# Kernel tuning notes

Hardware: AMD Instinct MI355X
Metric: run time of the kernel (lower is better)

The kernel has to match this reference:

```python
import jax, jax.numpy as jnp
import numpy as np

C_IN = 256
C_INTER = 128  # in_channels // reduction
B, H, W = 8, 64, 64


def setup_inputs() -> dict:
    key = jax.random.key(0)
    ks = jax.random.split(key, 9)
    s_in = 1.0 / np.sqrt(C_IN)
    s_int = 1.0 / np.sqrt(C_INTER)
    return {
        "x": jax.random.normal(ks[0], (B, C_IN, H, W), dtype=jnp.float32),
        "Wg": jax.random.uniform(ks[1], (C_INTER, C_IN), jnp.float32, -s_in, s_in),
        "bg": jax.random.uniform(ks[2], (C_INTER,), jnp.float32, -s_in, s_in),
        "Wt": jax.random.uniform(ks[3], (C_INTER, C_IN), jnp.float32, -s_in, s_in),
        "bt": jax.random.uniform(ks[4], (C_INTER,), jnp.float32, -s_in, s_in),
        "Wp": jax.random.uniform(ks[5], (C_INTER, C_IN), jnp.float32, -s_in, s_in),
        "bp": jax.random.uniform(ks[6], (C_INTER,), jnp.float32, -s_in, s_in),
        "Wo": jax.random.uniform(ks[7], (C_IN, C_INTER), jnp.float32, -s_int, s_int),
        "bo": jax.random.uniform(ks[8], (C_IN,), jnp.float32, -s_int, s_int),
    }


def reference(x, Wg, bg, Wt, bt, Wp, bp, Wo, bo):
    n, C, h, w = x.shape
    xf = x.reshape(n, C, h * w)                      # [n, C, L]
    # 1x1 convs == per-pixel linear projections
    g = jnp.einsum('dc,ncl->nld', Wg, xf) + bg       # [n, L, ci]
    th = jnp.einsum('dc,ncl->nld', Wt, xf) + bt      # [n, L, ci]
    ph = jnp.einsum('dc,ncl->ndl', Wp, xf) + bp[:, None]  # [n, ci, L]
    # embedded gaussian attention: softmax(theta @ phi) @ g
    scores = jnp.einsum('nld,ndm->nlm', th, ph)      # [n, L, L]
    attn = jax.nn.softmax(scores, axis=-1)
    y = jnp.einsum('nlm,nmd->nld', attn, g)          # [n, L, ci]
    out = jnp.einsum('cd,nld->ncl', Wo, y) + bo[None, :, None]  # [n, C, L]
    return out.reshape(n, C, h, w) + x
```

## Files before the change

kernel.cpp:

```cpp
#include <hip/hip_runtime.h>
#include <hip/hip_bf16.h>

#define NB  8
#define CIN 256
#define CI  128
#define LPX 4096

typedef __attribute__((ext_vector_type(8))) short short8;
typedef __attribute__((ext_vector_type(4))) float f32x4;
typedef __attribute__((ext_vector_type(16))) float f32x16;

#define MFMA16(a,b,c) __builtin_amdgcn_mfma_f32_16x16x32_bf16((a),(b),(c),0,0,0)
#define MFMA32(a,b,c) __builtin_amdgcn_mfma_f32_32x32x16_bf16((a),(b),(c),0,0,0)

__device__ __forceinline__ unsigned cvtpk_bf16(float lo, float hi) {
  unsigned r;
  asm("v_cvt_pk_bf16_f32 %0, %1, %2" : "=v"(r) : "v"(lo), "v"(hi));
  return r;
}

__device__ __forceinline__ f32x16 zero16() {
  f32x16 v;
#pragma unroll
  for (int i = 0; i < 16; ++i) v[i] = 0.f;
  return v;
}

__global__ __launch_bounds__(256) void cvt_kernel(
    const float* __restrict__ Wt, const float* __restrict__ Wp,
    const float* __restrict__ Wg, const float* __restrict__ Wo,
    __hip_bfloat16* __restrict__ WB, __hip_bfloat16* __restrict__ WoB)
{
  int idx = blockIdx.x * 256 + threadIdx.x;
  for (int i = idx; i < 384 * 256 + 256 * 128; i += 256 * 256) {
    if (i < 384 * 256) {
      float v = (i < 32768) ? Wt[i] : (i < 65536) ? Wp[i - 32768] : Wg[i - 65536];
      WB[i] = __float2bfloat16(v);
    } else {
      int j = i - 384 * 256;
      WoB[j] = __float2bfloat16(Wo[j]);
    }
  }
}

__global__ __launch_bounds__(256) void proj_kernel(
    const float* __restrict__ x,
    const __hip_bfloat16* __restrict__ WB,
    const float* __restrict__ bt, const float* __restrict__ bp,
    const float* __restrict__ bg,
    __hip_bfloat16* __restrict__ Q, __hip_bfloat16* __restrict__ Kv,
    __hip_bfloat16* __restrict__ VT)
{
  alignas(16) __shared__ __hip_bfloat16 xT[64][264];
  alignas(16) __shared__ __hip_bfloat16 vst[64][136];
  const int bid = blockIdx.x;
  const int n = bid >> 6, lt = bid & 63, l0 = lt * 64;
  const int t = threadIdx.x;

  const float* xn = x + (size_t)n * CIN * LPX;
  for (int idx = t; idx < CIN * 64; idx += 256) {
    int c = idx >> 6, l = idx & 63;
    xT[l][c] = __float2bfloat16(xn[(size_t)c * LPX + l0 + l]);
  }
  __syncthreads();

  const int w = t >> 6, lane = t & 63, fr = lane & 15, fq = lane >> 4;

  short8 af[8];
#pragma unroll
  for (int ks = 0; ks < 8; ++ks)
    af[ks] = *(const short8*)&xT[w * 16 + fr][ks * 32 + fq * 8];

  for (int dt = 0; dt < 24; ++dt) {
    int dl = (dt & 7) * 16 + fr;
    float bb = (dt < 8) ? bt[dl] : (dt < 16) ? bp[dl] : bg[dl];
    f32x4 acc = { bb, bb, bb, bb };
#pragma unroll
    for (int ks = 0; ks < 8; ++ks) {
      short8 bf = *(const short8*)&WB[(size_t)(dt * 16 + fr) * CIN + ks * 32 + fq * 8];
      acc = MFMA16(af[ks], bf, acc);
    }
    if (dt < 16) {
      __hip_bfloat16* dst = (dt < 8) ? Q : Kv;
#pragma unroll
      for (int r = 0; r < 4; ++r) {
        int l = l0 + w * 16 + fq * 4 + r;
        dst[((size_t)n * LPX + l) * CI + dl] = __float2bfloat16(acc[r]);
      }
    } else {
#pragma unroll
      for (int r = 0; r < 4; ++r)
        vst[w * 16 + fq * 4 + r][dl] = __float2bfloat16(acc[r]);
    }
  }
  __syncthreads();
#pragma unroll
  for (int iter = 0; iter < 32; ++iter) {
    int dv = (t >> 6) * 32 + iter;
    int lc = t & 63;
    VT[((size_t)n * CI + dv) * LPX + l0 + lc] = vst[lc][dv];
  }
}

struct KVBuf {
  __hip_bfloat16 Kl[64][136];
  __hip_bfloat16 Vl[128][72];
};

__global__ __launch_bounds__(256, 2) void attn_kernel(
    const __hip_bfloat16* __restrict__ Q, const __hip_bfloat16* __restrict__ Kv,
    const __hip_bfloat16* __restrict__ VT, const __hip_bfloat16* __restrict__ WoB,
    const float* __restrict__ bo, const float* __restrict__ x,
    float* __restrict__ out)
{
  alignas(16) __shared__ KVBuf bufs[2];
  __shared__ float rbuf[2][2][32];

  const int bid = blockIdx.x;
  const int n = bid >> 6, qt = bid & 63, l0 = qt * 64;
  const int t = threadIdx.x;
  const int w = t >> 6, lane = t & 63;
  const int l5 = lane & 31, hi = lane >> 5;
  const int wq = w >> 1, wm = w & 1;

  const __hip_bfloat16* Qn = Q  + (size_t)n * LPX * CI;
  const __hip_bfloat16* Kn = Kv + (size_t)n * LPX * CI;
  const __hip_bfloat16* Vn = VT + (size_t)n * CI * LPX;

  short8 qa[8];
#pragma unroll
  for (int ks = 0; ks < 8; ++ks)
    qa[ks] = *(const short8*)&Qn[(size_t)(l0 + wq * 32 + l5) * CI + ks * 16 + hi * 8];

  f32x16 yacc[4];
#pragma unroll
  for (int d = 0; d < 4; ++d) yacc[d] = zero16();
  float runl = 0.f;

  const int krow = t >> 2, kseg = t & 3;
  const int vrow = t >> 1, vseg = t & 1;
  uint4 kr[4], vr[4];

#define LOADKV(M0) do {                                                        \
    const uint4* sk_ = (const uint4*)&Kn[(size_t)((M0) + krow) * CI + kseg*32];\
    kr[0]=sk_[0]; kr[1]=sk_[1]; kr[2]=sk_[2]; kr[3]=sk_[3];                    \
    const uint4* sv_ = (const uint4*)&Vn[(size_t)vrow * LPX + (M0) + vseg*32]; \
    vr[0]=sv_[0]; vr[1]=sv_[1]; vr[2]=sv_[2]; vr[3]=sv_[3];                    \
  } while(0)

#define WRITEKV(B) do {                                                        \
    *(uint4*)&(B)->Kl[krow][kseg*32]      = kr[0];                             \
    *(uint4*)&(B)->Kl[krow][kseg*32 + 8]  = kr[1];                             \
    *(uint4*)&(B)->Kl[krow][kseg*32 + 16] = kr[2];                             \
    *(uint4*)&(B)->Kl[krow][kseg*32 + 24] = kr[3];                             \
    *(uint4*)&(B)->Vl[vrow][vseg*32]      = vr[0];                             \
    *(uint4*)&(B)->Vl[vrow][vseg*32 + 8]  = vr[1];                             \
    *(uint4*)&(B)->Vl[vrow][vseg*32 + 16] = vr[2];                             \
    *(uint4*)&(B)->Vl[vrow][vseg*32 + 24] = vr[3];                             \
  } while(0)

  LOADKV(0);
  WRITEKV(&bufs[0]);

  for (int it = 0; it < 64; ++it) {
    __syncthreads();
    KVBuf* cb = &bufs[it & 1];
    if (it < 63) LOADKV((it + 1) * 64);

    f32x16 sT = zero16();
#pragma unroll
    for (int ks = 0; ks < 8; ++ks) {
      short8 kf = *(const short8*)&cb->Kl[wm * 32 + l5][ks * 16 + hi * 8];
      sT = MFMA32(kf, qa[ks], sT);
    }

    float p[16];
#pragma unroll
    for (int r = 0; r < 16; ++r) { p[r] = __expf(sT[r]); runl += p[r]; }

#pragma unroll
    for (int mstep = 0; mstep < 2; ++mstep) {
      const int g = mstep * 8;
      unsigned a0 = cvtpk_bf16(p[g + 0], p[g + 1]);
      unsigned a1 = cvtpk_bf16(p[g + 2], p[g + 3]);
      unsigned b0 = cvtpk_bf16(p[g + 4], p[g + 5]);
      unsigned b1 = cvtpk_bf16(p[g + 6], p[g + 7]);
      unsigned sa0 = (unsigned)__shfl_xor((int)a0, 32);
      unsigned sa1 = (unsigned)__shfl_xor((int)a1, 32);
      unsigned sb0 = (unsigned)__shfl_xor((int)b0, 32);
      unsigned sb1 = (unsigned)__shfl_xor((int)b1, 32);
      union { unsigned u[4]; short8 s; } pk;
      pk.u[0] = hi ? sb0 : a0;
      pk.u[1] = hi ? sb1 : a1;
      pk.u[2] = hi ? b0  : sa0;
      pk.u[3] = hi ? b1  : sa1;
#pragma unroll
      for (int dblk = 0; dblk < 4; ++dblk) {
        short8 vf = *(const short8*)&cb->Vl[dblk * 32 + l5]
                                         [wm * 32 + mstep * 16 + hi * 8];
        yacc[dblk] = MFMA32(pk.s, vf, yacc[dblk]);
      }
    }

    if (it < 63) WRITEKV(&bufs[(it + 1) & 1]);
  }

  __syncthreads();

  runl += __shfl_xor(runl, 32);
  if (lane < 32) rbuf[wm][wq][lane] = runl;

  float* ys = (float*)&bufs[0];
  if (wm == 1) {
#pragma unroll
    for (int dblk = 0; dblk < 4; ++dblk)
#pragma unroll
      for (int r = 0; r < 16; ++r) {
        int row = (r & 3) + 8 * (r >> 2) + 4 * hi;
        ys[(size_t)(wq * 32 + row) * 128 + dblk * 32 + l5] = yacc[dblk][r];
      }
  }
  __syncthreads();

  __hip_bfloat16* yl = (__hip_bfloat16*)&bufs[1];
  if (wm == 0) {
#pragma unroll
    for (int r = 0; r < 16; ++r) {
      int row = (r & 3) + 8 * (r >> 2) + 4 * hi;
      float iv = 1.0f / (rbuf[0][wq][row] + rbuf[1][wq][row]);
#pragma unroll
      for (int dblk = 0; dblk < 4; ++dblk) {
        float v = yacc[dblk][r] +
                  ys[(size_t)(wq * 32 + row) * 128 + dblk * 32 + l5];
        yl[(size_t)(wq * 32 + row) * 136 + dblk * 32 + l5] = __float2bfloat16(v * iv);
      }
    }
  }
  __syncthreads();

  const int fr = lane & 15, fq = lane >> 4;
  for (int ct = 0; ct < 16; ++ct) {
    f32x4 o = f32x4{0.f, 0.f, 0.f, 0.f};
#pragma unroll
    for (int ks = 0; ks < 4; ++ks) {
      short8 wf = *(const short8*)&WoB[(size_t)(ct * 16 + fr) * CI + ks * 32 + fq * 8];
      short8 yf = *(const short8*)&yl[(size_t)(w * 16 + fr) * 136 + ks * 32 + fq * 8];
      o = MFMA16(wf, yf, o);
    }
#pragma unroll
    for (int r = 0; r < 4; ++r) {
      int c = ct * 16 + fq * 4 + r;
      size_t gi = ((size_t)n * CIN + c) * LPX + l0 + w * 16 + fr;
      out[gi] = o[r] + bo[c] + x[gi];
    }
  }
#undef LOADKV
#undef WRITEKV
}

extern "C" void kernel_launch(void* const* d_in, const int* in_sizes, int n_in,
                              void* d_out, int out_size, void* d_ws, size_t ws_size,
                              hipStream_t stream) {
  const float* x  = (const float*)d_in[0];
  const float* Wg = (const float*)d_in[1];
  const float* bg = (const float*)d_in[2];
  const float* Wt = (const float*)d_in[3];
  const float* bt = (const float*)d_in[4];
  const float* Wp = (const float*)d_in[5];
  const float* bp = (const float*)d_in[6];
  const float* Wo = (const float*)d_in[7];
  const float* bo = (const float*)d_in[8];
  float* out = (float*)d_out;

  char* ws = (char*)d_ws;
  const size_t SZ = (size_t)NB * LPX * CI * 2;
  __hip_bfloat16* Q   = (__hip_bfloat16*)(ws);
  __hip_bfloat16* Kv  = (__hip_bfloat16*)(ws + SZ);
  __hip_bfloat16* VT  = (__hip_bfloat16*)(ws + 2 * SZ);
  __hip_bfloat16* WB  = (__hip_bfloat16*)(ws + 3 * SZ);
  __hip_bfloat16* WoB = (__hip_bfloat16*)(ws + 3 * SZ + 384 * 256 * 2);

  cvt_kernel<<<256, 256, 0, stream>>>(Wt, Wp, Wg, Wo, WB, WoB);
  proj_kernel<<<512, 256, 0, stream>>>(x, WB, bt, bp, bg, Q, Kv, VT);
  attn_kernel<<<512, 256, 0, stream>>>(Q, Kv, VT, WoB, bo, x, out);
}
```

Measured before the change: 246.5 us.

## Load K/V fragments directly from global into registers, drop LDS staging

The attention loop stops staging K and V tiles through double-buffered shared memory with a barrier per iteration. Each wave now loads its MFMA fragments straight from global memory, splitting the key range in half between the two wm waves and prefetching the next K fragments in registers. The block index mapping is also swizzled so consecutive blocks cover different batches. This removes barriers and LDS traffic but makes each wave issue its own global (L2) loads. The wave pairs sharing a wq no longer reuse each other's K/V, so global load volume rises and V loads are strided by row.

```diff
diff --git a/kernel.cpp b/kernel.cpp
--- a/kernel.cpp
+++ b/kernel.cpp
@@ -102,22 +102,18 @@
   }
 }
 
-struct KVBuf {
-  __hip_bfloat16 Kl[64][136];
-  __hip_bfloat16 Vl[128][72];
-};
-
 __global__ __launch_bounds__(256, 2) void attn_kernel(
     const __hip_bfloat16* __restrict__ Q, const __hip_bfloat16* __restrict__ Kv,
     const __hip_bfloat16* __restrict__ VT, const __hip_bfloat16* __restrict__ WoB,
     const float* __restrict__ bo, const float* __restrict__ x,
     float* __restrict__ out)
 {
-  alignas(16) __shared__ KVBuf bufs[2];
+  alignas(16) __shared__ float ys[64][128];
+  alignas(16) __shared__ __hip_bfloat16 yl[64][136];
   __shared__ float rbuf[2][2][32];
 
   const int bid = blockIdx.x;
-  const int n = bid >> 6, qt = bid & 63, l0 = qt * 64;
+  const int n = bid & 7, qt = bid >> 3, l0 = qt * 64;
   const int t = threadIdx.x;
   const int w = t >> 6, lane = t & 63;
   const int l5 = lane & 31, hi = lane >> 5;
@@ -137,41 +133,33 @@
   for (int d = 0; d < 4; ++d) yacc[d] = zero16();
   float runl = 0.f;
 
-  const int krow = t >> 2, kseg = t & 3;
-  const int vrow = t >> 1, vseg = t & 1;
-  uint4 kr[4], vr[4];
-
-#define LOADKV(M0) do {                                                        \
-    const uint4* sk_ = (const uint4*)&Kn[(size_t)((M0) + krow) * CI + kseg*32];\
-    kr[0]=sk_[0]; kr[1]=sk_[1]; kr[2]=sk_[2]; kr[3]=sk_[3];                    \
-    const uint4* sv_ = (const uint4*)&Vn[(size_t)vrow * LPX + (M0) + vseg*32]; \
-    vr[0]=sv_[0]; vr[1]=sv_[1]; vr[2]=sv_[2]; vr[3]=sv_[3];                    \
-  } while(0)
-
-#define WRITEKV(B) do {                                                        \
-    *(uint4*)&(B)->Kl[krow][kseg*32]      = kr[0];                             \
-    *(uint4*)&(B)->Kl[krow][kseg*32 + 8]  = kr[1];                             \
-    *(uint4*)&(B)->Kl[krow][kseg*32 + 16] = kr[2];                             \
-    *(uint4*)&(B)->Kl[krow][kseg*32 + 24] = kr[3];                             \
-    *(uint4*)&(B)->Vl[vrow][vseg*32]      = vr[0];                             \
-    *(uint4*)&(B)->Vl[vrow][vseg*32 + 8]  = vr[1];                             \
-    *(uint4*)&(B)->Vl[vrow][vseg*32 + 16] = vr[2];                             \
-    *(uint4*)&(B)->Vl[vrow][vseg*32 + 24] = vr[3];                             \
-  } while(0)
-
-  LOADKV(0);
-  WRITEKV(&bufs[0]);
+  const int mbase = wm * 2048;
+
+  short8 kfc[8], kfn[8], vf[8];
+#pragma unroll
+  for (int ks = 0; ks < 8; ++ks)
+    kfc[ks] = *(const short8*)&Kn[(size_t)(mbase + l5) * CI + ks * 16 + hi * 8];
 
   for (int it = 0; it < 64; ++it) {
-    __syncthreads();
-    KVBuf* cb = &bufs[it & 1];
-    if (it < 63) LOADKV((it + 1) * 64);
+    const int m0 = mbase + it * 32;
+
+#pragma unroll
+    for (int mstep = 0; mstep < 2; ++mstep)
+#pragma unroll
+      for (int dblk = 0; dblk < 4; ++dblk)
+        vf[mstep * 4 + dblk] = *(const short8*)
+          &Vn[(size_t)(dblk * 32 + l5) * LPX + m0 + mstep * 16 + hi * 8];
 
     f32x16 sT = zero16();
 #pragma unroll
-    for (int ks = 0; ks < 8; ++ks) {
-      short8 kf = *(const short8*)&cb->Kl[wm * 32 + l5][ks * 16 + hi * 8];
-      sT = MFMA32(kf, qa[ks], sT);
+    for (int ks = 0; ks < 8; ++ks)
+      sT = MFMA32(kfc[ks], qa[ks], sT);
+
+    if (it < 63) {
+#pragma unroll
+      for (int ks = 0; ks < 8; ++ks)
+        kfn[ks] = *(const short8*)
+          &Kn[(size_t)(m0 + 32 + l5) * CI + ks * 16 + hi * 8];
     }
 
     float p[16];
@@ -195,34 +183,27 @@
       pk.u[2] = hi ? b0  : sa0;
       pk.u[3] = hi ? b1  : sa1;
 #pragma unroll
-      for (int dblk = 0; dblk < 4; ++dblk) {
-        short8 vf = *(const short8*)&cb->Vl[dblk * 32 + l5]
-                                         [wm * 32 + mstep * 16 + hi * 8];
-        yacc[dblk] = MFMA32(pk.s, vf, yacc[dblk]);
-      }
-    }
-
-    if (it < 63) WRITEKV(&bufs[(it + 1) & 1]);
-  }
-
-  __syncthreads();
+      for (int dblk = 0; dblk < 4; ++dblk)
+        yacc[dblk] = MFMA32(pk.s, vf[mstep * 4 + dblk], yacc[dblk]);
+    }
+
+#pragma unroll
+    for (int ks = 0; ks < 8; ++ks) kfc[ks] = kfn[ks];
+  }
 
   runl += __shfl_xor(runl, 32);
   if (lane < 32) rbuf[wm][wq][lane] = runl;
-
-  float* ys = (float*)&bufs[0];
   if (wm == 1) {
 #pragma unroll
     for (int dblk = 0; dblk < 4; ++dblk)
 #pragma unroll
       for (int r = 0; r < 16; ++r) {
         int row = (r & 3) + 8 * (r >> 2) + 4 * hi;
-        ys[(size_t)(wq * 32 + row) * 128 + dblk * 32 + l5] = yacc[dblk][r];
+        ys[wq * 32 + row][dblk * 32 + l5] = yacc[dblk][r];
       }
   }
   __syncthreads();
 
-  __hip_bfloat16* yl = (__hip_bfloat16*)&bufs[1];
   if (wm == 0) {
 #pragma unroll
     for (int r = 0; r < 16; ++r) {
@@ -230,9 +211,8 @@
       float iv = 1.0f / (rbuf[0][wq][row] + rbuf[1][wq][row]);
 #pragma unroll
       for (int dblk = 0; dblk < 4; ++dblk) {
-        float v = yacc[dblk][r] +
-                  ys[(size_t)(wq * 32 + row) * 128 + dblk * 32 + l5];
-        yl[(size_t)(wq * 32 + row) * 136 + dblk * 32 + l5] = __float2bfloat16(v * iv);
+        float v = yacc[dblk][r] + ys[wq * 32 + row][dblk * 32 + l5];
+        yl[wq * 32 + row][dblk * 32 + l5] = __float2bfloat16(v * iv);
       }
     }
   }
@@ -244,7 +224,7 @@
 #pragma unroll
     for (int ks = 0; ks < 4; ++ks) {
       short8 wf = *(const short8*)&WoB[(size_t)(ct * 16 + fr) * CI + ks * 32 + fq * 8];
-      short8 yf = *(const short8*)&yl[(size_t)(w * 16 + fr) * 136 + ks * 32 + fq * 8];
+      short8 yf = *(const short8*)&yl[w * 16 + fr][ks * 32 + fq * 8];
       o = MFMA16(wf, yf, o);
     }
 #pragma unroll
@@ -254,8 +234,6 @@
       out[gi] = o[r] + bo[c] + x[gi];
     }
   }
-#undef LOADKV
-#undef WRITEKV
 }
 
 extern "C" void kernel_launch(void* const* d_in, const int* in_sizes, int n_in,
```

After: 387.3 us. 1.57x slower.
